# Performance work log

Measured on AMD Instinct MI355X. Metric: run time of the kernel, lower is better.

Reference implementation:

```python
import jax, jax.numpy as jnp
import numpy as np

N, C, H, W = 8, 256, 31, 31
HIDDEN, OUT = 512, 256


def setup_inputs() -> dict:
    key = jax.random.key(0)
    k0, k1, k2, k3, k4 = jax.random.split(key, 5)
    x = jax.random.normal(k0, (N, C, H, W), dtype=jnp.float32)
    # Linear params (torch nn.Linear layout: [out_features, in_features])
    W1 = jax.random.normal(k1, (HIDDEN, C), dtype=jnp.float32) * (1.0 / np.sqrt(C))
    b1 = jax.random.normal(k2, (HIDDEN,), dtype=jnp.float32) * 0.01
    W2 = jax.random.normal(k3, (OUT, HIDDEN), dtype=jnp.float32) * (1.0 / np.sqrt(HIDDEN))
    b2 = jax.random.normal(k4, (OUT,), dtype=jnp.float32) * 0.01
    return {"x": x, "W1": W1, "b1": b1, "W2": W2, "b2": b2}


def _normalized_adjacency(n, h, w):
    M = n * h * w
    idx = jnp.arange(M)
    blk = idx // (h * w)          # sample id of each node
    pos = idx % (h * w)           # spatial position within sample
    # block-diagonal all-ones per sample
    same_block = (blk[:, None] == blk[None, :]).astype(jnp.float32)
    # identity link between consecutive samples (disjoint from block-diag)
    neighbor = ((jnp.abs(blk[:, None] - blk[None, :]) == 1)
                & (pos[:, None] == pos[None, :])).astype(jnp.float32)
    A = same_block + neighbor + jnp.eye(M, dtype=jnp.float32)
    deg = A.sum(axis=1)
    dinv = jnp.where(deg > 0, deg ** -0.5, 0.0)
    return A * dinv[:, None] * dinv[None, :]  # D^-1/2 A D^-1/2


def reference(x, W1, b1, W2, b2):
    n, c, h, w = x.shape
    weight = _normalized_adjacency(n, h, w)                 # [M, M]
    nodes = x.transpose(0, 2, 3, 1).reshape(-1, c)          # [M, C]
    hid = jax.nn.leaky_relu(weight @ nodes @ W1.T + b1)     # [M, HIDDEN]
    hid = jax.nn.leaky_relu(weight @ hid @ W2.T + b2)       # [M, OUT]
    hid = hid.reshape(n, h, w, -1).transpose(0, 3, 1, 2)    # [N, OUT, H, W]
    return hid.max(axis=0, keepdims=True)                   # [1, OUT, H, W]
```

## Files before the change

### kernel.cpp

```cpp
#include <hip/hip_runtime.h>
#include <math.h>

#define NS   8
#define CC   256
#define PP   961
#define MM   7688
#define MP   7744
#define HID  512
#define OUTC 256

typedef _Float16 h16;
using half8   = __attribute__((ext_vector_type(8))) _Float16;
using floatx4 = __attribute__((ext_vector_type(4))) float;

#define AS1 __attribute__((address_space(1)))
#define AS3 __attribute__((address_space(3)))

__device__ __forceinline__ float dinv_of(int b) {
    return (b == 0 || b == NS - 1) ? 0.0322245515f : 0.0322078318f;
}

__global__ void prep(const float* __restrict__ W1, const float* __restrict__ W2,
                     h16* __restrict__ w1h, h16* __restrict__ w2h,
                     const float* __restrict__ x, float* __restrict__ S1,
                     float* __restrict__ S2) {
    int blk = blockIdx.x, tid = threadIdx.x;
    if (blk < 256) {
        bool second = blk >= 128;
        const float* src = second ? W2 : W1;
        h16* dst = second ? w2h : w1h;
        int i = ((blk & 127) * 256 + tid) * 4;
        float4 v = *(const float4*)(src + i);
        dst[i + 0] = (h16)v.x; dst[i + 1] = (h16)v.y;
        dst[i + 2] = (h16)v.z; dst[i + 3] = (h16)v.w;
    } else if (blk < 2304) {
        int bc = blk - 256;
        const float* src = x + (size_t)bc * PP;
        float s = 0.f;
        for (int i = tid; i < PP; i += 256) s += src[i];
        __shared__ float red[256];
        red[tid] = s;
        __syncthreads();
        for (int off = 128; off > 0; off >>= 1) {
            if (tid < off) red[tid] += red[tid + off];
            __syncthreads();
        }
        if (tid == 0) S1[bc] = red[0];
    } else {
        int i = (blk - 2304) * 256 + tid;
        S2[i] = 0.f;
    }
}

__global__ void build_g1(const float* __restrict__ x, const float* __restrict__ S1,
                         h16* __restrict__ G1) {
    int pt = blockIdx.x, ct = blockIdx.y, b = blockIdx.z;
    int p0 = pt * 32, c0 = ct * 32;
    float db  = dinv_of(b);
    float wm  = (b > 0)      ? db * dinv_of(b - 1) : 0.f;
    float wp  = (b < NS - 1) ? db * dinv_of(b + 1) : 0.f;
    float db2 = db * db;
    __shared__ float t[32][33];
    int j = threadIdx.x & 31, i0 = threadIdx.x >> 5;
    int p = p0 + j;
    bool pv = (p < PP);
    #pragma unroll
    for (int r = 0; r < 4; ++r) {
        int i = i0 + r * 8;
        int c = c0 + i;
        float v = 0.f;
        if (pv) {
            size_t base = ((size_t)b * CC + c) * PP + p;
            float xb = x[base];
            float xm = (b > 0)      ? x[base - (size_t)CC * PP] : 0.f;
            float xp = (b < NS - 1) ? x[base + (size_t)CC * PP] : 0.f;
            v = db2 * (S1[b * CC + c] + xb) + wm * xm + wp * xp;
        }
        t[i][j] = v;
    }
    __syncthreads();
    int ii = threadIdx.x & 31, jj0 = threadIdx.x >> 5;
    #pragma unroll
    for (int r = 0; r < 4; ++r) {
        int jj = jj0 + r * 8;
        int pw = p0 + jj;
        if (pw < PP)
            G1[((size_t)b * PP + pw) * CC + c0 + ii] = (h16)t[ii][jj];
    }
}

template<int KD, bool DO_SUM, typename OutT>
__global__ __launch_bounds__(256) void mfma_gemm(
    const h16* __restrict__ A,
    const h16* __restrict__ B,
    const float* __restrict__ bias,
    OutT* __restrict__ C,
    float* __restrict__ S2,
    int M, int Nc)
{
    __shared__ __align__(16) h16 As[64 * 64];
    __shared__ __align__(16) h16 Bs[64 * 64];
    int tid = threadIdx.x, wave = tid >> 6, lane = tid & 63;
    int m0 = blockIdx.x * 64, n0 = blockIdx.y * 64;
    int sro = lane >> 3;
    int sch = (lane & 7) ^ sro;
    const h16* ga0 = A + (size_t)(m0 + wave * 16 + sro) * KD + sch * 8;
    const h16* gb0 = B + (size_t)(n0 + wave * 16 + sro) * KD + sch * 8;
    h16* la0 = &As[(wave * 16) * 64];
    h16* la1 = &As[(wave * 16 + 8) * 64];
    h16* lb0 = &Bs[(wave * 16) * 64];
    h16* lb1 = &Bs[(wave * 16 + 8) * 64];
    int fr = lane & 15, fq = lane >> 4;
    floatx4 acc[4] = {{0.f,0.f,0.f,0.f},{0.f,0.f,0.f,0.f},{0.f,0.f,0.f,0.f},{0.f,0.f,0.f,0.f}};
    for (int kk = 0; kk < KD; kk += 64) {
        __builtin_amdgcn_global_load_lds((const AS1 void*)(const void*)(ga0 + kk),
                                         (AS3 void*)(void*)la0, 16, 0, 0);
        __builtin_amdgcn_global_load_lds((const AS1 void*)(const void*)(ga0 + 8 * KD + kk),
                                         (AS3 void*)(void*)la1, 16, 0, 0);
        __builtin_amdgcn_global_load_lds((const AS1 void*)(const void*)(gb0 + kk),
                                         (AS3 void*)(void*)lb0, 16, 0, 0);
        __builtin_amdgcn_global_load_lds((const AS1 void*)(const void*)(gb0 + 8 * KD + kk),
                                         (AS3 void*)(void*)lb1, 16, 0, 0);
        __syncthreads();
        #pragma unroll
        for (int ks = 0; ks < 2; ++ks) {
            int slot = (ks * 4 + fq) ^ (fr & 7);
            half8 bf = *(const half8*)&Bs[(wave * 16 + fr) * 64 + slot * 8];
            #pragma unroll
            for (int mb = 0; mb < 4; ++mb) {
                half8 af = *(const half8*)&As[(mb * 16 + fr) * 64 + slot * 8];
                acc[mb] = __builtin_amdgcn_mfma_f32_16x16x32_f16(af, bf, acc[mb], 0, 0, 0);
            }
        }
        __syncthreads();
    }
    int col = n0 + wave * 16 + fr;
    float bv = bias[col];
    float s_lo = 0.f, s_hi = 0.f;
    int blo = m0 / 961;
    int mcut = (blo + 1) * 961;
    #pragma unroll
    for (int mb = 0; mb < 4; ++mb) {
        #pragma unroll
        for (int r = 0; r < 4; ++r) {
            int m = m0 + mb * 16 + fq * 4 + r;
            if (m < M) {
                float v = acc[mb][r] + bv;
                v = (v >= 0.f) ? v : 0.01f * v;
                C[(size_t)m * Nc + col] = (OutT)v;
                if (DO_SUM) { if (m < mcut) s_lo += v; else s_hi += v; }
            }
        }
    }
    if (DO_SUM) {
        s_lo += __shfl_xor(s_lo, 16);
        s_lo += __shfl_xor(s_lo, 32);
        s_hi += __shfl_xor(s_hi, 16);
        s_hi += __shfl_xor(s_hi, 32);
        if (fq == 0) {
            atomicAdd(&S2[blo * Nc + col], s_lo);
            int bhi = (m0 + 63) / 961;
            if (bhi != blo && bhi < NS) atomicAdd(&S2[bhi * Nc + col], s_hi);
        }
    }
}

__global__ void build_g2(const h16* __restrict__ H1, const float* __restrict__ S2,
                         h16* __restrict__ G2) {
    int id8 = blockIdx.x * 256 + threadIdx.x;
    int m = id8 >> 6;
    int h0 = (id8 & 63) * 8;
    int b = m / PP;
    float db = dinv_of(b);
    float dm = (b > 0)      ? dinv_of(b - 1) : 0.f;
    float dp = (b < NS - 1) ? dinv_of(b + 1) : 0.f;
    size_t base = (size_t)m * HID + h0;
    half8 z = {(h16)0,(h16)0,(h16)0,(h16)0,(h16)0,(h16)0,(h16)0,(h16)0};
    half8 hb = *(const half8*)(H1 + base);
    half8 hm = (b > 0)      ? *(const half8*)(H1 + base - (size_t)PP * HID) : z;
    half8 hp = (b < NS - 1) ? *(const half8*)(H1 + base + (size_t)PP * HID) : z;
    half8 o;
    #pragma unroll
    for (int j = 0; j < 8; ++j) {
        float v = db * (S2[b * HID + h0 + j] + (float)hb[j])
                + dm * (float)hm[j] + dp * (float)hp[j];
        o[j] = (h16)(db * v);
    }
    *(half8*)(G2 + base) = o;
}

__global__ void max_out(const float* __restrict__ H2, float* __restrict__ out) {
    int pt = blockIdx.x, ot = blockIdx.y;
    int p0 = pt * 32, o0 = ot * 32;
    __shared__ float t[32][33];
    int i = threadIdx.x & 31, j0 = threadIdx.x >> 5;
    #pragma unroll
    for (int r = 0; r < 4; ++r) {
        int j = j0 + r * 8;
        int p = p0 + j;
        float v = -INFINITY;
        if (p < PP) {
            #pragma unroll
            for (int b = 0; b < NS; ++b)
                v = fmaxf(v, H2[((size_t)b * PP + p) * OUTC + o0 + i]);
        }
        t[j][i] = v;
    }
    __syncthreads();
    int jj = threadIdx.x & 31, ii0 = threadIdx.x >> 5;
    #pragma unroll
    for (int r = 0; r < 4; ++r) {
        int ii = ii0 + r * 8;
        int pw = p0 + jj;
        if (pw < PP)
            out[(size_t)(o0 + ii) * PP + pw] = t[jj][ii];
    }
}

extern "C" void kernel_launch(void* const* d_in, const int* in_sizes, int n_in,
                              void* d_out, int out_size, void* d_ws, size_t ws_size,
                              hipStream_t stream) {
    const float* x  = (const float*)d_in[0];
    const float* W1 = (const float*)d_in[1];
    const float* b1 = (const float*)d_in[2];
    const float* W2 = (const float*)d_in[3];
    const float* b2 = (const float*)d_in[4];
    float* out = (float*)d_out;
    float* ws  = (float*)d_ws;

    float* S1  = ws;
    float* S2  = ws + 2048;
    h16*  w1h  = (h16*)(ws + 6144);
    h16*  w2h  = (h16*)(ws + 71680);
    h16*  G1   = (h16*)(ws + 137216);
    h16*  H1   = (h16*)(ws + 1128448);
    h16*  G2   = (h16*)(ws + 3096576);
    float* H2  = ws + 5079040;

    prep<<<2320, 256, 0, stream>>>(W1, W2, w1h, w2h, x, S1, S2);
    build_g1<<<dim3(31, 8, NS), 256, 0, stream>>>(x, S1, G1);
    mfma_gemm<CC, true, h16><<<dim3(MP / 64, HID / 64), 256, 0, stream>>>(
        G1, w1h, b1, H1, S2, MM, HID);
    build_g2<<<1922, 256, 0, stream>>>(H1, S2, G2);
    mfma_gemm<HID, false, float><<<dim3(MP / 64, OUTC / 64), 256, 0, stream>>>(
        G2, w2h, b2, H2, nullptr, MM, OUTC);
    max_out<<<dim3(31, 8), 256, 0, stream>>>(H2, out);
}
```

Baseline: 100.7 us.

## Reassociate second graph aggregation after W2 projection and fuse into max kernel

The second layer now multiplies H1 by W2 first, producing a 256-wide Y, and applies the structured adjacency (per-sample sums plus neighbour links) afterwards. The per-sample column sums move into the second GEMM's epilogue via atomics, and bias, leaky ReLU and the batch max move into the final kernel. This removes the build_g2 pass over the 512-wide hidden tensor and the G2 buffer, so the adjacency work runs on half as many columns. In exchange the second GEMM carries atomic sum work, and rounding order changes because the H1 sums are now taken after the fp32 projection.

```diff
diff --git a/kernel.cpp b/kernel.cpp
--- a/kernel.cpp
+++ b/kernel.cpp
@@ -23,7 +23,7 @@
 __global__ void prep(const float* __restrict__ W1, const float* __restrict__ W2,
                      h16* __restrict__ w1h, h16* __restrict__ w2h,
                      const float* __restrict__ x, float* __restrict__ S1,
-                     float* __restrict__ S2) {
+                     float* __restrict__ SY) {
     int blk = blockIdx.x, tid = threadIdx.x;
     if (blk < 256) {
         bool second = blk >= 128;
@@ -48,7 +48,7 @@
         if (tid == 0) S1[bc] = red[0];
     } else {
         int i = (blk - 2304) * 256 + tid;
-        S2[i] = 0.f;
+        SY[i] = 0.f;
     }
 }
 
@@ -89,13 +89,13 @@
     }
 }
 
-template<int KD, bool DO_SUM, typename OutT>
+template<int KD, bool ACT, bool DO_SUM, typename OutT>
 __global__ __launch_bounds__(256) void mfma_gemm(
     const h16* __restrict__ A,
     const h16* __restrict__ B,
     const float* __restrict__ bias,
     OutT* __restrict__ C,
-    float* __restrict__ S2,
+    float* __restrict__ SY,
     int M, int Nc)
 {
     __shared__ __align__(16) h16 As[64 * 64];
@@ -135,7 +135,7 @@
         __syncthreads();
     }
     int col = n0 + wave * 16 + fr;
-    float bv = bias[col];
+    float bv = ACT ? bias[col] : 0.f;
     float s_lo = 0.f, s_hi = 0.f;
     int blo = m0 / 961;
     int mcut = (blo + 1) * 961;
@@ -146,7 +146,7 @@
             int m = m0 + mb * 16 + fq * 4 + r;
             if (m < M) {
                 float v = acc[mb][r] + bv;
-                v = (v >= 0.f) ? v : 0.01f * v;
+                if (ACT) v = (v >= 0.f) ? v : 0.01f * v;
                 C[(size_t)m * Nc + col] = (OutT)v;
                 if (DO_SUM) { if (m < mcut) s_lo += v; else s_hi += v; }
             }
@@ -158,53 +158,43 @@
         s_hi += __shfl_xor(s_hi, 16);
         s_hi += __shfl_xor(s_hi, 32);
         if (fq == 0) {
-            atomicAdd(&S2[blo * Nc + col], s_lo);
+            atomicAdd(&SY[blo * Nc + col], s_lo);
             int bhi = (m0 + 63) / 961;
-            if (bhi != blo && bhi < NS) atomicAdd(&S2[bhi * Nc + col], s_hi);
-        }
-    }
-}
-
-__global__ void build_g2(const h16* __restrict__ H1, const float* __restrict__ S2,
-                         h16* __restrict__ G2) {
-    int id8 = blockIdx.x * 256 + threadIdx.x;
-    int m = id8 >> 6;
-    int h0 = (id8 & 63) * 8;
-    int b = m / PP;
-    float db = dinv_of(b);
-    float dm = (b > 0)      ? dinv_of(b - 1) : 0.f;
-    float dp = (b < NS - 1) ? dinv_of(b + 1) : 0.f;
-    size_t base = (size_t)m * HID + h0;
-    half8 z = {(h16)0,(h16)0,(h16)0,(h16)0,(h16)0,(h16)0,(h16)0,(h16)0};
-    half8 hb = *(const half8*)(H1 + base);
-    half8 hm = (b > 0)      ? *(const half8*)(H1 + base - (size_t)PP * HID) : z;
-    half8 hp = (b < NS - 1) ? *(const half8*)(H1 + base + (size_t)PP * HID) : z;
-    half8 o;
-    #pragma unroll
-    for (int j = 0; j < 8; ++j) {
-        float v = db * (S2[b * HID + h0 + j] + (float)hb[j])
-                + dm * (float)hm[j] + dp * (float)hp[j];
-        o[j] = (h16)(db * v);
-    }
-    *(half8*)(G2 + base) = o;
-}
-
-__global__ void max_out(const float* __restrict__ H2, float* __restrict__ out) {
+            if (bhi != blo && bhi < NS) atomicAdd(&SY[bhi * Nc + col], s_hi);
+        }
+    }
+}
+
+__global__ void final_max(const float* __restrict__ Y, const float* __restrict__ SY,
+                          const float* __restrict__ b2, float* __restrict__ out) {
     int pt = blockIdx.x, ot = blockIdx.y;
     int p0 = pt * 32, o0 = ot * 32;
     __shared__ float t[32][33];
     int i = threadIdx.x & 31, j0 = threadIdx.x >> 5;
+    int o = o0 + i;
+    float bias = b2[o];
     #pragma unroll
     for (int r = 0; r < 4; ++r) {
         int j = j0 + r * 8;
         int p = p0 + j;
-        float v = -INFINITY;
+        float vmax = -INFINITY;
         if (p < PP) {
+            float y[NS];
             #pragma unroll
             for (int b = 0; b < NS; ++b)
-                v = fmaxf(v, H2[((size_t)b * PP + p) * OUTC + o0 + i]);
-        }
-        t[j][i] = v;
+                y[b] = Y[((size_t)b * PP + p) * OUTC + o];
+            #pragma unroll
+            for (int b = 0; b < NS; ++b) {
+                float db = dinv_of(b);
+                float a = db * (SY[b * OUTC + o] + y[b]);
+                if (b > 0)      a += dinv_of(b - 1) * y[b - 1];
+                if (b < NS - 1) a += dinv_of(b + 1) * y[b + 1];
+                float z = db * a + bias;
+                z = (z >= 0.f) ? z : 0.01f * z;
+                vmax = fmaxf(vmax, z);
+            }
+        }
+        t[j][i] = vmax;
     }
     __syncthreads();
     int jj = threadIdx.x & 31, ii0 = threadIdx.x >> 5;
@@ -229,20 +219,18 @@
     float* ws  = (float*)d_ws;
 
     float* S1  = ws;
-    float* S2  = ws + 2048;
-    h16*  w1h  = (h16*)(ws + 6144);
-    h16*  w2h  = (h16*)(ws + 71680);
-    h16*  G1   = (h16*)(ws + 137216);
-    h16*  H1   = (h16*)(ws + 1128448);
-    h16*  G2   = (h16*)(ws + 3096576);
-    float* H2  = ws + 5079040;
-
-    prep<<<2320, 256, 0, stream>>>(W1, W2, w1h, w2h, x, S1, S2);
+    float* SY  = ws + 2048;
+    h16*  w1h  = (h16*)(ws + 4096);
+    h16*  w2h  = (h16*)(ws + 69632);
+    h16*  G1   = (h16*)(ws + 135168);
+    h16*  H1   = (h16*)(ws + 1126400);
+    float* Y   = ws + 3108864;
+
+    prep<<<2312, 256, 0, stream>>>(W1, W2, w1h, w2h, x, S1, SY);
     build_g1<<<dim3(31, 8, NS), 256, 0, stream>>>(x, S1, G1);
-    mfma_gemm<CC, true, h16><<<dim3(MP / 64, HID / 64), 256, 0, stream>>>(
-        G1, w1h, b1, H1, S2, MM, HID);
-    build_g2<<<1922, 256, 0, stream>>>(H1, S2, G2);
-    mfma_gemm<HID, false, float><<<dim3(MP / 64, OUTC / 64), 256, 0, stream>>>(
-        G2, w2h, b2, H2, nullptr, MM, OUTC);
-    max_out<<<dim3(31, 8), 256, 0, stream>>>(H2, out);
-}
+    mfma_gemm<CC, true, false, h16><<<dim3(MP / 64, HID / 64), 256, 0, stream>>>(
+        G1, w1h, b1, H1, nullptr, MM, HID);
+    mfma_gemm<HID, false, true, float><<<dim3(MP / 64, OUTC / 64), 256, 0, stream>>>(
+        H1, w2h, nullptr, Y, SY, MM, OUTC);
+    final_max<<<dim3(31, 8), 256, 0, stream>>>(Y, SY, b2, out);
+}
```

After: 95.41 us. -5.2%, faster.
